# Kernel optimization log

Measured on AMD Instinct MI355X. Metric: run time of the kernel, lower is better.

Reference implementation:

```python
import jax, jax.numpy as jnp
import numpy as np

T, B, E = 2048, 16, 1024   # time, batch, embed_dim (fairseq T x B x C layout)
CDIM = 1024                # conv_dim
H = 16                     # num_heads
K = 31                     # kernel_size, padding_l = K-1 (causal left pad)


def _xavier(k, shape):
    fan_out, fan_in = shape
    lim = float(np.sqrt(6.0 / (fan_in + fan_out)))
    return jax.random.uniform(k, shape, jnp.float32, -lim, lim)


def setup_inputs() -> dict:
    key = jax.random.key(0)
    ks = jax.random.split(key, 5)
    return {
        "x": jax.random.normal(ks[0], (T, B, E), jnp.float32),
        "w1": _xavier(ks[1], (CDIM, E)),
        "b1": jnp.zeros((CDIM,), jnp.float32),
        "ww": _xavier(ks[2], (H * K, CDIM)),  # DynamicConv weight_linear
        "bw": jnp.zeros((H * K,), jnp.float32),
        "w2": _xavier(ks[3], (E, CDIM)),
        "b2": jnp.zeros((E,), jnp.float32),
        "gamma": jnp.ones((E,), jnp.float32),
        "beta": jnp.zeros((E,), jnp.float32),
    }


def layer_norm(x, g, b, eps=1e-5):
    m = x.mean(-1, keepdims=True)
    v = ((x - m) ** 2).mean(-1, keepdims=True)
    return (x - m) * jax.lax.rsqrt(v + eps) * g + b


def dynamic_conv(h, ww, bw):
    # h: [T, B, C]; per-position softmax kernel weights shared across R=C/H channels per head
    Tn, Bn, C = h.shape
    R = C // H
    w = jax.nn.softmax((h @ ww.T + bw).reshape(Tn, Bn, H, K), axis=-1)  # [T,B,H,K]
    hp = jnp.pad(h.reshape(Tn, Bn, H, R), ((K - 1, 0), (0, 0), (0, 0), (0, 0)))
    # out[t] = sum_k w[t,:,:,k] * h[t + k - (K-1)]  (causal banded aggregation)
    acc = jnp.zeros((Tn, Bn, H, R), h.dtype)
    for k in range(K):  # fixed small kernel-size loop, not a data-dim loop
        acc = acc + w[:, :, :, k:k + 1] * hp[k:k + Tn]
    return acc.reshape(Tn, Bn, C)


def reference(x, w1, b1, ww, bw, w2, b2, gamma, beta):
    # eval mode: all dropouts are identity; normalize_before=False -> LN after residual
    h = x @ w1.T + b1            # linear1: [T,B,E] -> [T,B,CDIM]
    h = dynamic_conv(h, ww, bw)  # DynamicConv, weight_softmax=True, no conv bias
    h = h @ w2.T + b2            # linear2: back to embed_dim
    return layer_norm(x + h, gamma, beta)
```

## Files before the change

### kernel.cpp

```cpp
#include <hip/hip_runtime.h>

#define T_DIM 2048
#define B_DIM 16
#define E_DIM 1024
#define CD    1024
#define NH    16
#define KSZ   31
#define M_DIM 32768
#define SLICE 131072
#define BSTRIDE 2097152

typedef unsigned int u32;
typedef unsigned short u16;
typedef __attribute__((ext_vector_type(8))) __bf16 bf16x8;
typedef __attribute__((ext_vector_type(4))) float f32x4;
typedef __attribute__((ext_vector_type(4))) float fvec4;
typedef __attribute__((ext_vector_type(8))) unsigned short us8;
typedef __attribute__((ext_vector_type(4))) unsigned short us4;
typedef __attribute__((ext_vector_type(4))) unsigned int ui4;

__device__ __forceinline__ float bf2f(u16 u) {
  union { float f; u32 i; } c; c.i = ((u32)u) << 16; return c.f;
}
__device__ __forceinline__ u16 f2bf(float f) {
  union { float f; u32 i; } c; c.f = f;
  u32 u = c.i;
  u += 0x7fffu + ((u >> 16) & 1u);
  return (u16)(u >> 16);
}

#define GLDS(gp, lp)                                                        \
  __builtin_amdgcn_global_load_lds(                                         \
      (__attribute__((address_space(1))) void*)(gp),                        \
      (__attribute__((address_space(3))) void*)(lp), 16, 0, 0)

__global__ __launch_bounds__(256) void zfill(u16* __restrict__ z) {
  ((ui4*)z)[threadIdx.x] = (ui4)(0u);
}

__global__ __launch_bounds__(256) void cvt_f32_bf16(const float* __restrict__ src,
                                                    u16* __restrict__ dst, int n4) {
  int i = blockIdx.x * 256 + threadIdx.x;
  int stride = gridDim.x * 256;
  const fvec4* s4 = (const fvec4*)src;
  us4* d4 = (us4*)dst;
  for (; i < n4; i += stride) {
    fvec4 v = s4[i];
    us4 o;
    o[0] = f2bf(v[0]); o[1] = f2bf(v[1]); o[2] = f2bf(v[2]); o[3] = f2bf(v[3]);
    d4[i] = o;
  }
}

template<int OUT_MODE, int GUARD_N, int A_MODE>
__global__ __launch_bounds__(512, 2) void gemm256(
    const void* __restrict__ Av, const u16* __restrict__ B,
    const float* __restrict__ bias, void* __restrict__ Cout,
    int N, int K, int ldc, int ntn)
{
  __shared__ u16 sA[2][256 * 64];
  __shared__ u16 sB[2][256 * 64];
  const int tid = threadIdx.x;
  const int lane = tid & 63;
  const int wid = tid >> 6;
  const int wr = wid >> 2;
  const int wc = wid & 3;

  const int swz = (blockIdx.x & 7) * (gridDim.x >> 3) + (blockIdx.x >> 3);
  const int bm = (swz / ntn) * 256;
  const int bn = (swz % ntn) * 256;

  const int srow = tid >> 3;
  const int scol = (tid & 7) * 8;
  const int scols = scol ^ ((srow & 7) << 3);
  const int sdst   = srow * 64 + scol;
  const int sdst_s = srow * 64 + scols;

  const u16* Ab = (const u16*)Av;
  const float* Af = (const float*)Av;

  const u16* gA[4];
  const float* gX[4];
  #pragma unroll
  for (int st = 0; st < 4; st++) {
    int rr = bm + st * 64 + srow;
    if (A_MODE == 1) {
      gA[st] = Ab + (size_t)(rr >> 11) * BSTRIDE + (size_t)(rr & 2047) * 64 + scols;
      gX[st] = nullptr;
    } else {
      int t = rr & 2047, b = rr >> 11;
      gX[st] = Af + (size_t)(t * 16 + b) * 1024 + scol;
      gA[st] = nullptr;
    }
  }
  const u16* gB[4];
  #pragma unroll
  for (int st = 0; st < 4; st++) {
    int br = bn + st * 64 + srow;
    if (GUARD_N) br = min(br, N - 1);
    gB[st] = B + (size_t)br * K + scols;
  }

  f32x4 acc[8][4];
  #pragma unroll
  for (int i = 0; i < 8; i++)
    #pragma unroll
    for (int j = 0; j < 4; j++) acc[i][j] = (f32x4)(0.0f);

  const int fr = lane & 15;
  const int g8 = (lane >> 4) * 8;
  const int sx = (fr & 7) << 3;

  const int NT = K >> 6;
  int buf = 0;

  #pragma unroll
  for (int st = 0; st < 4; st++) GLDS(gB[st], &sB[0][st * 4096 + sdst]);
  if (A_MODE == 1) {
    #pragma unroll
    for (int st = 0; st < 4; st++) GLDS(gA[st], &sA[0][st * 4096 + sdst]);
    asm volatile("s_waitcnt vmcnt(0)" ::: "memory");
  } else {
    fvec4 q[4][2];
    #pragma unroll
    for (int st = 0; st < 4; st++) {
      q[st][0] = *(const fvec4*)(gX[st]);
      q[st][1] = *(const fvec4*)(gX[st] + 4);
    }
    #pragma unroll
    for (int st = 0; st < 4; st++) {
      us8 o;
      #pragma unroll
      for (int e = 0; e < 4; e++) { o[e] = f2bf(q[st][0][e]); o[e + 4] = f2bf(q[st][1][e]); }
      *(us8*)&sA[0][st * 4096 + sdst_s] = o;
    }
    asm volatile("s_waitcnt vmcnt(0)" ::: "memory");
    asm volatile("s_waitcnt lgkmcnt(0)" ::: "memory");
  }
  __builtin_amdgcn_s_barrier();

  for (int kt = 0; kt < NT; kt++) {
    const bool more = (kt + 1 < NT);
    const size_t koB = (size_t)(kt + 1) * 64;
    const size_t koA = (size_t)(kt + 1) * SLICE;
    const size_t koX = (size_t)(kt + 1) * 64;
    u16* dA = &sA[buf ^ 1][0];
    u16* dB = &sB[buf ^ 1][0];
    fvec4 xa[4][2];

    bf16x8 bF[4][2];
    #pragma unroll
    for (int n = 0; n < 4; n++)
      #pragma unroll
      for (int kh = 0; kh < 2; kh++) {
        int row = wc * 64 + n * 16 + fr;
        bF[n][kh] = *(const bf16x8*)&sB[buf][row * 64 + ((kh * 32 + g8) ^ sx)];
      }
    bf16x8 aF[2][2];
    #pragma unroll
    for (int mi = 0; mi < 2; mi++)
      #pragma unroll
      for (int kh = 0; kh < 2; kh++) {
        int row = wr * 128 + mi * 16 + fr;
        aF[mi][kh] = *(const bf16x8*)&sA[buf][row * 64 + ((kh * 32 + g8) ^ sx)];
      }
    if (more) {
      GLDS(gB[0] + koB, dB + 0 * 4096 + sdst);
      GLDS(gB[1] + koB, dB + 1 * 4096 + sdst);
      if (A_MODE == 2) {
        xa[0][0] = *(const fvec4*)(gX[0] + koX); xa[0][1] = *(const fvec4*)(gX[0] + koX + 4);
        xa[1][0] = *(const fvec4*)(gX[1] + koX); xa[1][1] = *(const fvec4*)(gX[1] + koX + 4);
      }
    }
    __builtin_amdgcn_s_barrier();
    asm volatile("s_waitcnt lgkmcnt(0)" ::: "memory");
    __builtin_amdgcn_sched_barrier(0);
    __builtin_amdgcn_s_setprio(1);
    #pragma unroll
    for (int mi = 0; mi < 2; mi++)
      #pragma unroll
      for (int n = 0; n < 4; n++)
        #pragma unroll
        for (int kh = 0; kh < 2; kh++)
          acc[mi][n] = __builtin_amdgcn_mfma_f32_16x16x32_bf16(aF[mi][kh], bF[n][kh], acc[mi][n], 0, 0, 0);
    __builtin_amdgcn_s_setprio(0);
    __builtin_amdgcn_sched_barrier(0);
    __builtin_amdgcn_s_barrier();

    {
      bf16x8 aG[2][2];
      #pragma unroll
      for (int mi = 0; mi < 2; mi++)
        #pragma unroll
        for (int kh = 0; kh < 2; kh++) {
          int row = wr * 128 + (2 + mi) * 16 + fr;
          aG[mi][kh] = *(const bf16x8*)&sA[buf][row * 64 + ((kh * 32 + g8) ^ sx)];
        }
      if (more) {
        GLDS(gB[2] + koB, dB + 2 * 4096 + sdst);
        GLDS(gB[3] + koB, dB + 3 * 4096 + sdst);
        if (A_MODE == 2) {
          xa[2][0] = *(const fvec4*)(gX[2] + koX); xa[2][1] = *(const fvec4*)(gX[2] + koX + 4);
          xa[3][0] = *(const fvec4*)(gX[3] + koX); xa[3][1] = *(const fvec4*)(gX[3] + koX + 4);
        }
      }
      __builtin_amdgcn_s_barrier();
      asm volatile("s_waitcnt lgkmcnt(0)" ::: "memory");
      __builtin_amdgcn_sched_barrier(0);
      __builtin_amdgcn_s_setprio(1);
      #pragma unroll
      for (int mi = 0; mi < 2; mi++)
        #pragma unroll
        for (int n = 0; n < 4; n++)
          #pragma unroll
          for (int kh = 0; kh < 2; kh++)
            acc[2 + mi][n] = __builtin_amdgcn_mfma_f32_16x16x32_bf16(aG[mi][kh], bF[n][kh], acc[2 + mi][n], 0, 0, 0);
      __builtin_amdgcn_s_setprio(0);
      __builtin_amdgcn_sched_barrier(0);
      if (A_MODE == 1) {
        if (more) { asm volatile("s_waitcnt vmcnt(4)" ::: "memory"); }
        else      { asm volatile("s_waitcnt vmcnt(0)" ::: "memory"); }
      }
      __builtin_amdgcn_s_barrier();
    }

    {
      bf16x8 aG[2][2];
      #pragma unroll
      for (int mi = 0; mi < 2; mi++)
        #pragma unroll
        for (int kh = 0; kh < 2; kh++) {
          int row = wr * 128 + (4 + mi) * 16 + fr;
          aG[mi][kh] = *(const bf16x8*)&sA[buf][row * 64 + ((kh * 32 + g8) ^ sx)];
        }
      if (more) {
        if (A_MODE == 1) {
          GLDS(gA[0] + koA, dA + 0 * 4096 + sdst);
          GLDS(gA[2] + koA, dA + 2 * 4096 + sdst);
        } else {
          #pragma unroll
          for (int st = 0; st < 2; st++) {
            us8 o;
            #pragma unroll
            for (int e = 0; e < 4; e++) { o[e] = f2bf(xa[st][0][e]); o[e + 4] = f2bf(xa[st][1][e]); }
            *(us8*)(dA + st * 4096 + sdst_s) = o;
          }
        }
      }
      __builtin_amdgcn_s_barrier();
      asm volatile("s_waitcnt lgkmcnt(0)" ::: "memory");
      __builtin_amdgcn_sched_barrier(0);
      __builtin_amdgcn_s_setprio(1);
      #pragma unroll
      for (int mi = 0; mi < 2; mi++)
        #pragma unroll
        for (int n = 0; n < 4; n++)
          #pragma unroll
          for (int kh = 0; kh < 2; kh++)
            acc[4 + mi][n] = __builtin_amdgcn_mfma_f32_16x16x32_bf16(aG[mi][kh], bF[n][kh], acc[4 + mi][n], 0, 0, 0);
      __builtin_amdgcn_s_setprio(0);
      __builtin_amdgcn_sched_barrier(0);
      __builtin_amdgcn_s_barrier();
    }

    {
      bf16x8 aG[2][2];
      #pragma unroll
      for (int mi = 0; mi < 2; mi++)
        #pragma unroll
        for (int kh = 0; kh < 2; kh++) {
          int row = wr * 128 + (6 + mi) * 16 + fr;
          aG[mi][kh] = *(const bf16x8*)&sA[buf][row * 64 + ((kh * 32 + g8) ^ sx)];
        }
      if (more) {
        if (A_MODE == 1) {
          GLDS(gA[1] + koA, dA + 1 * 4096 + sdst);
          GLDS(gA[3] + koA, dA + 3 * 4096 + sdst);
        } else {
          #pragma unroll
          for (int st = 2; st < 4; st++) {
            us8 o;
            #pragma unroll
            for (int e = 0; e < 4; e++) { o[e] = f2bf(xa[st][0][e]); o[e + 4] = f2bf(xa[st][1][e]); }
            *(us8*)(dA + st * 4096 + sdst_s) = o;
          }
        }
      }
      if (A_MODE == 2) {
        if (more) { asm volatile("s_waitcnt vmcnt(0)" ::: "memory"); }
        asm volatile("s_waitcnt lgkmcnt(0)" ::: "memory");
      }
      __builtin_amdgcn_s_barrier();
      asm volatile("s_waitcnt lgkmcnt(0)" ::: "memory");
      __builtin_amdgcn_sched_barrier(0);
      __builtin_amdgcn_s_setprio(1);
      #pragma unroll
      for (int mi = 0; mi < 2; mi++)
        #pragma unroll
        for (int n = 0; n < 4; n++)
          #pragma unroll
          for (int kh = 0; kh < 2; kh++)
            acc[6 + mi][n] = __builtin_amdgcn_mfma_f32_16x16x32_bf16(aG[mi][kh], bF[n][kh], acc[6 + mi][n], 0, 0, 0);
      __builtin_amdgcn_s_setprio(0);
      __builtin_amdgcn_sched_barrier(0);
      if (A_MODE == 1 && more) {
        asm volatile("s_waitcnt vmcnt(2)" ::: "memory");
      }
      __builtin_amdgcn_s_barrier();
    }
    buf ^= 1;
  }

  const int orow0 = bm + wr * 128 + (lane >> 4) * 4;
  const int ocol0 = bn + wc * 64 + fr;
  #pragma unroll
  for (int m = 0; m < 8; m++) {
    #pragma unroll
    for (int n = 0; n < 4; n++) {
      #pragma unroll
      for (int q = 0; q < 4; q++) {
        int row = orow0 + m * 16 + q;
        int col = ocol0 + n * 16;
        if (!GUARD_N || col < N) {
          float v = acc[m][n][q] + bias[col];
          if (OUT_MODE == 1) {
            ((u16*)Cout)[(size_t)row * ldc + col] = f2bf(v);
          } else if (OUT_MODE == 2) {
            int bb = row >> 11, t = row & 2047;
            int hh = col / 31, kk = col - hh * 31;
            ((u16*)Cout)[((size_t)((bb * NH + hh) * T_DIM + t)) * 32 + kk] = f2bf(v);
          } else {
            int bb = row >> 11, t = row & 2047;
            ((u16*)Cout)[(size_t)((bb << 4) + (col >> 6)) * SLICE + (size_t)t * 64 + (col & 63)] = f2bf(v);
          }
        }
      }
    }
  }
}

__global__ __launch_bounds__(256) void dconv(const u16* __restrict__ h1,
                                             const u16* __restrict__ wt,
                                             const u16* __restrict__ zreg,
                                             u16* __restrict__ outc)
{
  constexpr int TT = 64, HALO = 30, SW = 33;
  int bid = blockIdx.x;
  int tt = bid & 31;
  int s  = bid >> 5;
  int t0 = tt * TT;
  __shared__ u16 hl[96 * 64];
  __shared__ float wl[TT * SW];
  int tid = threadIdx.x;

  const u16* slice = h1 + (size_t)s * SLICE;
  #pragma unroll
  for (int it = 0; it < 3; it++) {
    int c = it * 256 + tid;
    int row = t0 - HALO + (c >> 3);
    const u16* src = slice + (size_t)row * 64 + (c & 7) * 8;
    if (row < 0) src = zreg + (c & 7) * 8;
    GLDS(src, hl + c * 8);
  }
  {
    const u16* wsrc = wt + ((size_t)s * T_DIM + t0) * 32;
    int j = tid * 8;
    us8 v = *(const us8*)(wsrc + j);
    int row = j >> 5, col = j & 31;
    #pragma unroll
    for (int e = 0; e < 8; e++) wl[row * SW + col + e] = bf2f(v[e]);
  }
  __syncthreads();

  if (tid < TT) {
    float* p = wl + tid * SW;
    float v[KSZ];
    float mx = -1e30f;
    #pragma unroll
    for (int k = 0; k < KSZ; k++) { v[k] = p[k]; mx = fmaxf(mx, v[k]); }
    float sum = 0.f;
    #pragma unroll
    for (int k = 0; k < KSZ; k++) { v[k] = __expf(v[k] - mx); sum += v[k]; }
    float inv = 1.0f / sum;
    #pragma unroll
    for (int k = 0; k < KSZ; k++) p[k] = v[k] * inv;
  }
  __syncthreads();

  int rb = (tid & 7) * 8;
  int tl = tid >> 3;

  #pragma unroll
  for (int half = 0; half < 2; half++) {
    const int tb = tl + half * 32;
    const float* wp = wl + tb * SW;
    const u16* hb = hl + tb * 64 + rb;
    float acc[8];
    #pragma unroll
    for (int e = 0; e < 8; e++) acc[e] = 0.f;
    #pragma unroll
    for (int k = 0; k < KSZ; k++) {
      us8 hv = *(const us8*)(hb + k * 64);
      float w = wp[k];
      #pragma unroll
      for (int e = 0; e < 8; e++) acc[e] += w * bf2f(hv[e]);
    }
    us8 o;
    #pragma unroll
    for (int e = 0; e < 8; e++) o[e] = f2bf(acc[e]);
    *(us8*)(outc + (size_t)s * SLICE + (size_t)(t0 + tb) * 64 + rb) = o;
  }
}

__global__ __launch_bounds__(256) void ln_res(const float* __restrict__ x,
                                              const u16* __restrict__ hb,
                                              float* __restrict__ out,
                                              const float* __restrict__ gamma,
                                              const float* __restrict__ beta)
{
  int mp = blockIdx.x;
  int b = mp >> 11, t = mp & 2047;
  int xrow = t * 16 + b;
  const fvec4* xr = (const fvec4*)(x + (size_t)xrow * E_DIM);
  const us4* hr = (const us4*)(hb + (size_t)mp * E_DIM);
  fvec4* yr = (fvec4*)(out + (size_t)xrow * E_DIM);
  int tid = threadIdx.x;
  us4 hv = hr[tid];
  fvec4 xv = xr[tid];
  fvec4 s;
  #pragma unroll
  for (int e = 0; e < 4; e++) s[e] = xv[e] + bf2f(hv[e]);
  float sum = s[0] + s[1] + s[2] + s[3];
  float sq  = s[0]*s[0] + s[1]*s[1] + s[2]*s[2] + s[3]*s[3];
  #pragma unroll
  for (int off = 32; off >= 1; off >>= 1) {
    sum += __shfl_xor(sum, off, 64);
    sq  += __shfl_xor(sq, off, 64);
  }
  __shared__ float red[8];
  int lane = tid & 63, wid = tid >> 6;
  if (lane == 0) { red[wid] = sum; red[4 + wid] = sq; }
  __syncthreads();
  sum = red[0] + red[1] + red[2] + red[3];
  sq  = red[4] + red[5] + red[6] + red[7];
  float mean = sum * (1.0f / E_DIM);
  float var  = sq * (1.0f / E_DIM) - mean * mean;
  float rstd = rsqrtf(var + 1e-5f);
  fvec4 g = ((const fvec4*)gamma)[tid];
  fvec4 be = ((const fvec4*)beta)[tid];
  fvec4 o;
  #pragma unroll
  for (int e = 0; e < 4; e++) o[e] = (s[e] - mean) * rstd * g[e] + be[e];
  yr[tid] = o;
}

extern "C" void kernel_launch(void* const* d_in, const int* in_sizes, int n_in,
                              void* d_out, int out_size, void* d_ws, size_t ws_size,
                              hipStream_t stream)
{
  const float* x     = (const float*)d_in[0];
  const float* w1    = (const float*)d_in[1];
  const float* b1    = (const float*)d_in[2];
  const float* ww    = (const float*)d_in[3];
  const float* bw    = (const float*)d_in[4];
  const float* w2    = (const float*)d_in[5];
  const float* b2    = (const float*)d_in[6];
  const float* gamma = (const float*)d_in[7];
  const float* beta  = (const float*)d_in[8];
  float* out = (float*)d_out;

  char* ws = (char*)d_ws;
  u16*   convp = (u16*)(ws);
  u16*   h1p  = (u16*)(ws + ((size_t)64 << 20));
  u16*   wt   = (u16*)(ws + ((size_t)128 << 20));
  u16*   w1b  = (u16*)(ws + ((size_t)192 << 20));
  u16*   w2b  = (u16*)(ws + ((size_t)194 << 20));
  u16*   wwb  = (u16*)(ws + ((size_t)196 << 20));
  u16*   zreg = (u16*)(ws + ((size_t)198 << 20));
  u16*   h2p  = h1p;

  zfill<<<1, 256, 0, stream>>>(zreg);
  cvt_f32_bf16<<<1024, 256, 0, stream>>>(w1, w1b, (CD * E_DIM) / 4);
  cvt_f32_bf16<<<1024, 256, 0, stream>>>(w2, w2b, (E_DIM * CD) / 4);
  cvt_f32_bf16<<<512,  256, 0, stream>>>(ww, wwb, (NH * KSZ * CD) / 4);

  gemm256<3, 0, 2><<<512, 512, 0, stream>>>(x, w1b, b1, h1p, CD, E_DIM, 0, 4);
  gemm256<2, 1, 1><<<256, 512, 0, stream>>>(h1p, wwb, bw, wt, NH * KSZ, CD, 0, 2);
  dconv<<<8192, 256, 0, stream>>>(h1p, wt, zreg, convp);
  gemm256<1, 0, 1><<<512, 512, 0, stream>>>(convp, w2b, b2, h2p, E_DIM, CD, E_DIM, 4);
  ln_res<<<32768, 256, 0, stream>>>(x, h2p, out, gamma, beta);
}
```

Baseline: 373.1 us.

## Pre-convert x to transposed bf16 in a fused prep kernel; use async LDS loads

Replaces the zero-fill and three weight-conversion launches with a single prep kernel. That kernel also converts x to bf16 in a batch-major layout. The first GEMM can then load A directly into LDS with global_load_lds instead of loading fp32 through registers, converting, and writing to LDS, which removes the extra vmcnt(0) stalls on that path. The cost is an extra pass over x: 128MB read and 64MB written before the GEMM. This traffic may outweigh the pipelining gain.

```diff
diff --git a/kernel.cpp b/kernel.cpp
--- a/kernel.cpp
+++ b/kernel.cpp
@@ -34,27 +34,54 @@
       (__attribute__((address_space(1))) void*)(gp),                        \
       (__attribute__((address_space(3))) void*)(lp), 16, 0, 0)
 
-__global__ __launch_bounds__(256) void zfill(u16* __restrict__ z) {
-  ((ui4*)z)[threadIdx.x] = (ui4)(0u);
-}
-
-__global__ __launch_bounds__(256) void cvt_f32_bf16(const float* __restrict__ src,
-                                                    u16* __restrict__ dst, int n4) {
+__global__ __launch_bounds__(256) void prep(const float* __restrict__ x,
+                                            const float* __restrict__ w1,
+                                            const float* __restrict__ w2,
+                                            const float* __restrict__ ww,
+                                            u16* __restrict__ xbt,
+                                            u16* __restrict__ w1b,
+                                            u16* __restrict__ w2b,
+                                            u16* __restrict__ wwb,
+                                            u16* __restrict__ zreg)
+{
+  const int NX = (T_DIM * B_DIM * E_DIM) / 4;
+  const int N1 = NX + (CD * E_DIM) / 4;
+  const int N2 = N1 + (E_DIM * CD) / 4;
+  const int N3 = N2 + (NH * KSZ * CD) / 4;
   int i = blockIdx.x * 256 + threadIdx.x;
-  int stride = gridDim.x * 256;
-  const fvec4* s4 = (const fvec4*)src;
-  us4* d4 = (us4*)dst;
-  for (; i < n4; i += stride) {
-    fvec4 v = s4[i];
+  if (i < NX) {
+    int rr = i >> 8, c = i & 255;
+    int t = rr >> 4, b = rr & 15;
+    fvec4 v = ((const fvec4*)x)[i];
     us4 o;
     o[0] = f2bf(v[0]); o[1] = f2bf(v[1]); o[2] = f2bf(v[2]); o[3] = f2bf(v[3]);
-    d4[i] = o;
-  }
-}
-
-template<int OUT_MODE, int GUARD_N, int A_MODE>
+    ((us4*)xbt)[(size_t)(b * T_DIM + t) * 256 + c] = o;
+  } else if (i < N1) {
+    int j = i - NX;
+    fvec4 v = ((const fvec4*)w1)[j];
+    us4 o;
+    o[0] = f2bf(v[0]); o[1] = f2bf(v[1]); o[2] = f2bf(v[2]); o[3] = f2bf(v[3]);
+    ((us4*)w1b)[j] = o;
+  } else if (i < N2) {
+    int j = i - N1;
+    fvec4 v = ((const fvec4*)w2)[j];
+    us4 o;
+    o[0] = f2bf(v[0]); o[1] = f2bf(v[1]); o[2] = f2bf(v[2]); o[3] = f2bf(v[3]);
+    ((us4*)w2b)[j] = o;
+  } else if (i < N3) {
+    int j = i - N2;
+    fvec4 v = ((const fvec4*)ww)[j];
+    us4 o;
+    o[0] = f2bf(v[0]); o[1] = f2bf(v[1]); o[2] = f2bf(v[2]); o[3] = f2bf(v[3]);
+    ((us4*)wwb)[j] = o;
+  } else {
+    ((ui4*)zreg)[i - N3] = (ui4)(0u);
+  }
+}
+
+template<int OUT_MODE, int GUARD_N, int A_CONV>
 __global__ __launch_bounds__(512, 2) void gemm256(
-    const void* __restrict__ Av, const u16* __restrict__ B,
+    const u16* __restrict__ A, const u16* __restrict__ B,
     const float* __restrict__ bias, void* __restrict__ Cout,
     int N, int K, int ldc, int ntn)
 {
@@ -73,25 +100,16 @@
   const int srow = tid >> 3;
   const int scol = (tid & 7) * 8;
   const int scols = scol ^ ((srow & 7) << 3);
-  const int sdst   = srow * 64 + scol;
-  const int sdst_s = srow * 64 + scols;
-
-  const u16* Ab = (const u16*)Av;
-  const float* Af = (const float*)Av;
+  const int sdst = srow * 64 + scol;
 
   const u16* gA[4];
-  const float* gX[4];
   #pragma unroll
   for (int st = 0; st < 4; st++) {
     int rr = bm + st * 64 + srow;
-    if (A_MODE == 1) {
-      gA[st] = Ab + (size_t)(rr >> 11) * BSTRIDE + (size_t)(rr & 2047) * 64 + scols;
-      gX[st] = nullptr;
-    } else {
-      int t = rr & 2047, b = rr >> 11;
-      gX[st] = Af + (size_t)(t * 16 + b) * 1024 + scol;
-      gA[st] = nullptr;
-    }
+    if (A_CONV)
+      gA[st] = A + (size_t)(rr >> 11) * BSTRIDE + (size_t)(rr & 2047) * 64 + scols;
+    else
+      gA[st] = A + (size_t)rr * K + scols;
   }
   const u16* gB[4];
   #pragma unroll
@@ -116,37 +134,17 @@
 
   #pragma unroll
   for (int st = 0; st < 4; st++) GLDS(gB[st], &sB[0][st * 4096 + sdst]);
-  if (A_MODE == 1) {
-    #pragma unroll
-    for (int st = 0; st < 4; st++) GLDS(gA[st], &sA[0][st * 4096 + sdst]);
-    asm volatile("s_waitcnt vmcnt(0)" ::: "memory");
-  } else {
-    fvec4 q[4][2];
-    #pragma unroll
-    for (int st = 0; st < 4; st++) {
-      q[st][0] = *(const fvec4*)(gX[st]);
-      q[st][1] = *(const fvec4*)(gX[st] + 4);
-    }
-    #pragma unroll
-    for (int st = 0; st < 4; st++) {
-      us8 o;
-      #pragma unroll
-      for (int e = 0; e < 4; e++) { o[e] = f2bf(q[st][0][e]); o[e + 4] = f2bf(q[st][1][e]); }
-      *(us8*)&sA[0][st * 4096 + sdst_s] = o;
-    }
-    asm volatile("s_waitcnt vmcnt(0)" ::: "memory");
-    asm volatile("s_waitcnt lgkmcnt(0)" ::: "memory");
-  }
+  #pragma unroll
+  for (int st = 0; st < 4; st++) GLDS(gA[st], &sA[0][st * 4096 + sdst]);
+  asm volatile("s_waitcnt vmcnt(0)" ::: "memory");
   __builtin_amdgcn_s_barrier();
 
   for (int kt = 0; kt < NT; kt++) {
     const bool more = (kt + 1 < NT);
+    const size_t koA = A_CONV ? (size_t)(kt + 1) * SLICE : (size_t)(kt + 1) * 64;
     const size_t koB = (size_t)(kt + 1) * 64;
-    const size_t koA = (size_t)(kt + 1) * SLICE;
-    const size_t koX = (size_t)(kt + 1) * 64;
     u16* dA = &sA[buf ^ 1][0];
     u16* dB = &sB[buf ^ 1][0];
-    fvec4 xa[4][2];
 
     bf16x8 bF[4][2];
     #pragma unroll
@@ -167,10 +165,6 @@
     if (more) {
       GLDS(gB[0] + koB, dB + 0 * 4096 + sdst);
       GLDS(gB[1] + koB, dB + 1 * 4096 + sdst);
-      if (A_MODE == 2) {
-        xa[0][0] = *(const fvec4*)(gX[0] + koX); xa[0][1] = *(const fvec4*)(gX[0] + koX + 4);
-        xa[1][0] = *(const fvec4*)(gX[1] + koX); xa[1][1] = *(const fvec4*)(gX[1] + koX + 4);
-      }
     }
     __builtin_amdgcn_s_barrier();
     asm volatile("s_waitcnt lgkmcnt(0)" ::: "memory");
@@ -199,10 +193,6 @@
       if (more) {
         GLDS(gB[2] + koB, dB + 2 * 4096 + sdst);
         GLDS(gB[3] + koB, dB + 3 * 4096 + sdst);
-        if (A_MODE == 2) {
-          xa[2][0] = *(const fvec4*)(gX[2] + koX); xa[2][1] = *(const fvec4*)(gX[2] + koX + 4);
-          xa[3][0] = *(const fvec4*)(gX[3] + koX); xa[3][1] = *(const fvec4*)(gX[3] + koX + 4);
-        }
       }
       __builtin_amdgcn_s_barrier();
       asm volatile("s_waitcnt lgkmcnt(0)" ::: "memory");
@@ -217,10 +207,8 @@
             acc[2 + mi][n] = __builtin_amdgcn_mfma_f32_16x16x32_bf16(aG[mi][kh], bF[n][kh], acc[2 + mi][n], 0, 0, 0);
       __builtin_amdgcn_s_setprio(0);
       __builtin_amdgcn_sched_barrier(0);
-      if (A_MODE == 1) {
-        if (more) { asm volatile("s_waitcnt vmcnt(4)" ::: "memory"); }
-        else      { asm volatile("s_waitcnt vmcnt(0)" ::: "memory"); }
-      }
+      if (more) { asm volatile("s_waitcnt vmcnt(4)" ::: "memory"); }
+      else      { asm volatile("s_waitcnt vmcnt(0)" ::: "memory"); }
       __builtin_amdgcn_s_barrier();
     }
 
@@ -234,18 +222,8 @@
           aG[mi][kh] = *(const bf16x8*)&sA[buf][row * 64 + ((kh * 32 + g8) ^ sx)];
         }
       if (more) {
-        if (A_MODE == 1) {
-          GLDS(gA[0] + koA, dA + 0 * 4096 + sdst);
-          GLDS(gA[2] + koA, dA + 2 * 4096 + sdst);
-        } else {
-          #pragma unroll
-          for (int st = 0; st < 2; st++) {
-            us8 o;
-            #pragma unroll
-            for (int e = 0; e < 4; e++) { o[e] = f2bf(xa[st][0][e]); o[e + 4] = f2bf(xa[st][1][e]); }
-            *(us8*)(dA + st * 4096 + sdst_s) = o;
-          }
-        }
+        GLDS(gA[0] + koA, dA + 0 * 4096 + sdst);
+        GLDS(gA[2] + koA, dA + 2 * 4096 + sdst);
       }
       __builtin_amdgcn_s_barrier();
       asm volatile("s_waitcnt lgkmcnt(0)" ::: "memory");
@@ -273,22 +251,8 @@
           aG[mi][kh] = *(const bf16x8*)&sA[buf][row * 64 + ((kh * 32 + g8) ^ sx)];
         }
       if (more) {
-        if (A_MODE == 1) {
-          GLDS(gA[1] + koA, dA + 1 * 4096 + sdst);
-          GLDS(gA[3] + koA, dA + 3 * 4096 + sdst);
-        } else {
-          #pragma unroll
-          for (int st = 2; st < 4; st++) {
-            us8 o;
-            #pragma unroll
-            for (int e = 0; e < 4; e++) { o[e] = f2bf(xa[st][0][e]); o[e + 4] = f2bf(xa[st][1][e]); }
-            *(us8*)(dA + st * 4096 + sdst_s) = o;
-          }
-        }
-      }
-      if (A_MODE == 2) {
-        if (more) { asm volatile("s_waitcnt vmcnt(0)" ::: "memory"); }
-        asm volatile("s_waitcnt lgkmcnt(0)" ::: "memory");
+        GLDS(gA[1] + koA, dA + 1 * 4096 + sdst);
+        GLDS(gA[3] + koA, dA + 3 * 4096 + sdst);
       }
       __builtin_amdgcn_s_barrier();
       asm volatile("s_waitcnt lgkmcnt(0)" ::: "memory");
@@ -303,7 +267,7 @@
             acc[6 + mi][n] = __builtin_amdgcn_mfma_f32_16x16x32_bf16(aG[mi][kh], bF[n][kh], acc[6 + mi][n], 0, 0, 0);
       __builtin_amdgcn_s_setprio(0);
       __builtin_amdgcn_sched_barrier(0);
-      if (A_MODE == 1 && more) {
+      if (more) {
         asm volatile("s_waitcnt vmcnt(2)" ::: "memory");
       }
       __builtin_amdgcn_s_barrier();
@@ -470,21 +434,19 @@
   float* out = (float*)d_out;
 
   char* ws = (char*)d_ws;
-  u16*   convp = (u16*)(ws);
+  u16*   xbt  = (u16*)(ws);
   u16*   h1p  = (u16*)(ws + ((size_t)64 << 20));
   u16*   wt   = (u16*)(ws + ((size_t)128 << 20));
   u16*   w1b  = (u16*)(ws + ((size_t)192 << 20));
   u16*   w2b  = (u16*)(ws + ((size_t)194 << 20));
   u16*   wwb  = (u16*)(ws + ((size_t)196 << 20));
   u16*   zreg = (u16*)(ws + ((size_t)198 << 20));
+  u16*   convp = xbt;
   u16*   h2p  = h1p;
 
-  zfill<<<1, 256, 0, stream>>>(zreg);
-  cvt_f32_bf16<<<1024, 256, 0, stream>>>(w1, w1b, (CD * E_DIM) / 4);
-  cvt_f32_bf16<<<1024, 256, 0, stream>>>(w2, w2b, (E_DIM * CD) / 4);
-  cvt_f32_bf16<<<512,  256, 0, stream>>>(ww, wwb, (NH * KSZ * CD) / 4);
-
-  gemm256<3, 0, 2><<<512, 512, 0, stream>>>(x, w1b, b1, h1p, CD, E_DIM, 0, 4);
+  prep<<<35313, 256, 0, stream>>>(x, w1, w2, ww, xbt, w1b, w2b, wwb, zreg);
+
+  gemm256<3, 0, 0><<<512, 512, 0, stream>>>(xbt, w1b, b1, h1p, CD, E_DIM, 0, 4);
   gemm256<2, 1, 1><<<256, 512, 0, stream>>>(h1p, wwb, bw, wt, NH * KSZ, CD, 0, 2);
   dconv<<<8192, 256, 0, stream>>>(h1p, wt, zreg, convp);
   gemm256<1, 0, 1><<<512, 512, 0, stream>>>(convp, w2b, b2, h2p, E_DIM, CD, E_DIM, 4);
```

Result: faster. 353.9 us (-5.2%).
